# Optimization experiments

Measured on AMD Instinct MI355X. Metric: run time of the kernel, lower is better.

The kernel has to match this reference:

```python
import jax, jax.numpy as jnp
import numpy as np

B, D, K = 32768, 256, 16  # batch, latent_dim, n_embeddings
COMMITMENT_COST = 0.25


def setup_inputs() -> dict:
    key = jax.random.key(0)
    k1, k2 = jax.random.split(key)
    z = jax.random.normal(k1, (B, D), dtype=jnp.float32)
    # torch init: uniform_(-1/n_embeddings, 1/n_embeddings), one scalar codebook per dim
    codebooks = jax.random.uniform(k2, (D, K), dtype=jnp.float32,
                                   minval=-1.0 / K, maxval=1.0 / K)
    return {"z": z, "codebooks": codebooks}


def reference(z, codebooks):
    # Vectorized over all D per-dimension codebooks at once.
    # distances[b, d, k] = (z[b, d] - codebooks[d, k])^2
    distances = (z[:, :, None] - codebooks[None, :, :]) ** 2  # (B, D, K)
    indices = jnp.argmin(distances, axis=-1)                  # (B, D) int
    # gather nearest scalar code per (sample, dim)
    z_q = codebooks[jnp.arange(D)[None, :], indices]          # (B, D)

    sg = jax.lax.stop_gradient
    # per-dim MSE (mean over batch), summed over dims — matches the python loop
    q_latent = jnp.sum(jnp.mean((z_q - sg(z)) ** 2, axis=0))
    e_latent = jnp.sum(jnp.mean((sg(z_q) - z) ** 2, axis=0))
    vq_loss = q_latent + COMMITMENT_COST * e_latent

    z_q_sg = z + sg(z_q - z)  # straight-through estimator
    return (z_q_sg, vq_loss, indices)
```

## Files before the change

### kernel.cpp

```cpp
#include <hip/hip_runtime.h>


constexpr int Bn = 32768;
constexpr int Dn = 256;
constexpr int Kn = 16;
constexpr int NQUAD = Bn * Dn / 4;
constexpr int GRID = 2048;
constexpr int BLOCK = 256;
constexpr int QPT = NQUAD / (GRID * BLOCK);
constexpr int ROWP = 260;
constexpr float LOSS_SCALE = 1.25f / (float)Bn;

__global__ void vq_init_loss(float* out) {
    if (threadIdx.x == 0) out[(size_t)Bn * Dn] = 0.0f;
}

__global__ __launch_bounds__(BLOCK) void vq_main(const float* __restrict__ z,
                                                 const float* __restrict__ cb,
                                                 float* __restrict__ out) {
    __shared__ float cbt[Kn * ROWP];
    __shared__ float wsum[4];
    for (int i = threadIdx.x; i < Kn * Dn; i += BLOCK) {
        int d = i >> 4;
        int k = i & (Kn - 1);
        cbt[k * ROWP + d] = cb[i];
    }
    __syncthreads();

    float* __restrict__ zq   = out;
    float* __restrict__ idxf = out + (size_t)Bn * Dn + 1;

    const int tid = blockIdx.x * BLOCK + threadIdx.x;
    const int stride = GRID * BLOCK;
    const int d0 = (tid * 4) & (Dn - 1);

    float4 zv[QPT];
    #pragma unroll
    for (int it = 0; it < QPT; ++it)
        zv[it] = *reinterpret_cast<const float4*>(z + (size_t)(tid + it * stride) * 4);

    float acc = 0.0f;
    #pragma unroll
    for (int it = 0; it < QPT; ++it) {
        const int f = (tid + it * stride) * 4;
        const float zz[4] = {zv[it].x, zv[it].y, zv[it].z, zv[it].w};

        float best[4] = {1e30f, 1e30f, 1e30f, 1e30f};
        int   bi[4]   = {0, 0, 0, 0};

        #pragma unroll
        for (int k = 0; k < Kn; ++k) {
            const float4 c = *reinterpret_cast<const float4*>(&cbt[k * ROWP + d0]);
            const float cc[4] = {c.x, c.y, c.z, c.w};
            #pragma unroll
            for (int j = 0; j < 4; ++j) {
                float dd = zz[j] - cc[j];
                float d2 = dd * dd;
                bi[j]   = (d2 < best[j]) ? k : bi[j];
                best[j] = fminf(best[j], d2);
            }
        }

        float bc[4];
        #pragma unroll
        for (int j = 0; j < 4; ++j)
            bc[j] = cbt[bi[j] * ROWP + d0 + j];

        *reinterpret_cast<float4*>(zq + f) = make_float4(bc[0], bc[1], bc[2], bc[3]);

        idxf[f + 0] = (float)bi[0];
        idxf[f + 1] = (float)bi[1];
        idxf[f + 2] = (float)bi[2];
        idxf[f + 3] = (float)bi[3];

        acc += best[0] + best[1] + best[2] + best[3];
    }

    #pragma unroll
    for (int off = 32; off > 0; off >>= 1)
        acc += __shfl_down(acc, off, 64);

    const int lane = threadIdx.x & 63;
    const int wid  = threadIdx.x >> 6;
    if (lane == 0) wsum[wid] = acc;
    __syncthreads();
    if (threadIdx.x == 0) {
        float s = (wsum[0] + wsum[1] + wsum[2] + wsum[3]) * LOSS_SCALE;
        atomicAdd(out + (size_t)Bn * Dn, s);
    }
}

extern "C" void kernel_launch(void* const* d_in, const int* in_sizes, int n_in,
                              void* d_out, int out_size, void* d_ws, size_t ws_size,
                              hipStream_t stream) {
    const float* z  = (const float*)d_in[0];
    const float* cb = (const float*)d_in[1];
    float* out = (float*)d_out;

    vq_init_loss<<<1, 64, 0, stream>>>(out);
    vq_main<<<GRID, BLOCK, 0, stream>>>(z, cb, out);
}
```

Baseline: 123.8 us.

## Double grid size, raise occupancy, vectorize codebook load, track best code inline

Doubles the grid so each thread handles two quads, and adds a minimum-blocks-per-SM hint to the launch bounds to raise occupancy. The codebook is now loaded into shared memory with float4 reads. The nearest code value is tracked in registers during the argmin loop, which removes the dependent shared-memory gather afterwards. The z loads are hardcoded to two quads, so the code silently assumes QPT equals 2. Doubling the grid also doubles per-block setup work and the number of loss atomics.

```diff
diff --git a/kernel.cpp b/kernel.cpp
--- a/kernel.cpp
+++ b/kernel.cpp
@@ -5,7 +5,7 @@
 constexpr int Dn = 256;
 constexpr int Kn = 16;
 constexpr int NQUAD = Bn * Dn / 4;
-constexpr int GRID = 2048;
+constexpr int GRID = 4096;
 constexpr int BLOCK = 256;
 constexpr int QPT = NQUAD / (GRID * BLOCK);
 constexpr int ROWP = 260;
@@ -15,15 +15,21 @@
     if (threadIdx.x == 0) out[(size_t)Bn * Dn] = 0.0f;
 }
 
-__global__ __launch_bounds__(BLOCK) void vq_main(const float* __restrict__ z,
-                                                 const float* __restrict__ cb,
-                                                 float* __restrict__ out) {
+__global__ __launch_bounds__(BLOCK, 8) void vq_main(const float* __restrict__ z,
+                                                    const float* __restrict__ cb,
+                                                    float* __restrict__ out) {
     __shared__ float cbt[Kn * ROWP];
     __shared__ float wsum[4];
-    for (int i = threadIdx.x; i < Kn * Dn; i += BLOCK) {
-        int d = i >> 4;
-        int k = i & (Kn - 1);
-        cbt[k * ROWP + d] = cb[i];
+    #pragma unroll
+    for (int it = 0; it < 4; ++it) {
+        const int i4 = threadIdx.x + it * BLOCK;
+        const float4 c4 = *reinterpret_cast<const float4*>(cb + i4 * 4);
+        const int d  = i4 >> 2;
+        const int k0 = (i4 & 3) * 4;
+        cbt[(k0 + 0) * ROWP + d] = c4.x;
+        cbt[(k0 + 1) * ROWP + d] = c4.y;
+        cbt[(k0 + 2) * ROWP + d] = c4.z;
+        cbt[(k0 + 3) * ROWP + d] = c4.w;
     }
     __syncthreads();
 
@@ -34,18 +40,18 @@
     const int stride = GRID * BLOCK;
     const int d0 = (tid * 4) & (Dn - 1);
 
-    float4 zv[QPT];
-    #pragma unroll
-    for (int it = 0; it < QPT; ++it)
-        zv[it] = *reinterpret_cast<const float4*>(z + (size_t)(tid + it * stride) * 4);
+    float4 zv0 = *reinterpret_cast<const float4*>(z + (size_t)tid * 4);
+    float4 zv1 = *reinterpret_cast<const float4*>(z + (size_t)(tid + stride) * 4);
 
     float acc = 0.0f;
     #pragma unroll
     for (int it = 0; it < QPT; ++it) {
         const int f = (tid + it * stride) * 4;
-        const float zz[4] = {zv[it].x, zv[it].y, zv[it].z, zv[it].w};
+        const float4 zv = (it == 0) ? zv0 : zv1;
+        const float zz[4] = {zv.x, zv.y, zv.z, zv.w};
 
         float best[4] = {1e30f, 1e30f, 1e30f, 1e30f};
+        float bc[4]   = {0.f, 0.f, 0.f, 0.f};
         int   bi[4]   = {0, 0, 0, 0};
 
         #pragma unroll
@@ -56,15 +62,12 @@
             for (int j = 0; j < 4; ++j) {
                 float dd = zz[j] - cc[j];
                 float d2 = dd * dd;
-                bi[j]   = (d2 < best[j]) ? k : bi[j];
-                best[j] = fminf(best[j], d2);
+                bool lt = d2 < best[j];
+                best[j] = lt ? d2 : best[j];
+                bc[j]   = lt ? cc[j] : bc[j];
+                bi[j]   = lt ? k : bi[j];
             }
         }
-
-        float bc[4];
-        #pragma unroll
-        for (int j = 0; j < 4; ++j)
-            bc[j] = cbt[bi[j] * ROWP + d0 + j];
 
         *reinterpret_cast<float4*>(zq + f) = make_float4(bc[0], bc[1], bc[2], bc[3]);
 
```

New measurement: 224.2 us. 81.1% more time.
